# Kernel tuning notes

Measured on AMD Instinct MI355X. Metric: run time of the kernel, lower is better.

The kernel has to match this reference:

```python
import jax, jax.numpy as jnp
import numpy as np

RES = 300          # grid resolution per axis
NC_D = 16          # density_n_comp
NC_A = 48          # app_n_comp
APP_DIM = 27       # app_dim
N = 500000         # number of ray samples

MAT_MODE = [[0, 1], [0, 2], [1, 2]]
VEC_MODE = [2, 1, 0]


def setup_inputs() -> dict:
    key = jax.random.key(0)
    k0, k1, k2, k3 = jax.random.split(key, 4)
    xyz_sampled = jax.random.uniform(k0, (N, 3), minval=-1.0, maxval=1.0, dtype=jnp.float32)
    plane_coef = 0.1 * jax.random.normal(k1, (3, NC_A + NC_D, RES, RES), dtype=jnp.float32)
    line_coef = 0.1 * jax.random.normal(k2, (3, NC_A + NC_D, RES, 1), dtype=jnp.float32)
    basis_W = jax.random.normal(k3, (APP_DIM, 3 * NC_A), dtype=jnp.float32) / np.sqrt(3 * NC_A)
    return {"xyz_sampled": xyz_sampled, "plane_coef": plane_coef,
            "line_coef": line_coef, "basis_W": basis_W}


def _grid_sample(img, x, y):
    """Bilinear grid_sample, align_corners=True, zeros padding.
    img: (C, H, W); x, y: (N,) normalized coords in [-1, 1] (x -> W, y -> H).
    Returns (C, N)."""
    C, H, W = img.shape
    ix = (x + 1.0) * 0.5 * (W - 1)
    iy = (y + 1.0) * 0.5 * (H - 1)
    x0f = jnp.floor(ix)
    y0f = jnp.floor(iy)
    wx = ix - x0f   # weight for x0+1
    wy = iy - y0f   # weight for y0+1
    x0 = x0f.astype(jnp.int32)
    y0 = y0f.astype(jnp.int32)
    out = jnp.zeros((C, x.shape[0]), img.dtype)
    for dx, wxc in ((0, 1.0 - wx), (1, wx)):
        for dy, wyc in ((0, 1.0 - wy), (1, wy)):
            xi = x0 + dx
            yi = y0 + dy
            valid = (xi >= 0) & (xi < W) & (yi >= 0) & (yi < H)
            xic = jnp.clip(xi, 0, W - 1)
            yic = jnp.clip(yi, 0, H - 1)
            w = jnp.where(valid, wxc * wyc, 0.0)
            out = out + img[:, yic, xic] * w
    return out


def reference(xyz_sampled, plane_coef, line_coef, basis_W):
    zeros = jnp.zeros((xyz_sampled.shape[0],), xyz_sampled.dtype)
    pf, lf = [], []
    for i in range(3):
        m0, m1 = MAT_MODE[i]
        # plane: grid = (x=xyz[m0] -> W, y=xyz[m1] -> H)
        pf.append(_grid_sample(plane_coef[i], xyz_sampled[:, m0], xyz_sampled[:, m1]))
        # line: grid = (x=0 -> W(=1), y=xyz[vecMode] -> H) => 1D interp along H
        lf.append(_grid_sample(line_coef[i], zeros, xyz_sampled[:, VEC_MODE[i]]))
    pf = jnp.stack(pf)  # (3, NC_A+NC_D, N)
    lf = jnp.stack(lf)  # (3, NC_A+NC_D, N)
    # compute_densityfeature: last density_n_comp channels, multiply and sum-reduce
    sigma_feature = jnp.sum(pf[:, NC_A:] * lf[:, NC_A:], axis=(0, 1))  # (N,)
    # compute_appfeature: first app_n_comp channels, multiply then basis projection
    app_feats = (pf[:, :NC_A] * lf[:, :NC_A]).reshape(3 * NC_A, -1)    # (3*NC_A, N)
    app_features = app_feats.T @ basis_W.T                              # (N, APP_DIM)
    return sigma_feature, app_features
```

## Files before the change

kernel.cpp:

```cpp
#include <hip/hip_runtime.h>
#include <hip/hip_bf16.h>

#define RES 300
#define NPLANE (RES * RES)
#define NC_A 48
#define APP_DIM 27
#define KDIM 144
#define KS 168

#define NPBLK 4219

__device__ __forceinline__ float bf_lo(unsigned int u) { return __uint_as_float(u << 16); }
__device__ __forceinline__ float bf_hi(unsigned int u) { return __uint_as_float(u & 0xffff0000u); }

__global__ __launch_bounds__(256) void prep(
    const float* __restrict__ plane, const float* __restrict__ line,
    const float* __restrict__ W,
    uint2* __restrict__ TpV, unsigned int* __restrict__ TlP,
    __hip_bfloat16* __restrict__ Wg) {
  __shared__ unsigned int ltile[64 * 65];
  const int blk = blockIdx.x;
  const int tid = threadIdx.x;

  if (blk < NPBLK) {
    int flat = blk * 256 + tid;
    if (flat < 1080000) {
      int c4   = flat & 15;
      int rest = flat >> 4;
      int i  = (rest >= 45000) ? 2 : (rest >= 22500 ? 1 : 0);
      int p0 = (rest - i * 22500) * 4;
      const float* src = plane + (size_t)(i * 64 + c4 * 4) * NPLANE + p0;
      float4 r0 = *(const float4*)(src);
      float4 r1 = *(const float4*)(src + NPLANE);
      float4 r2 = *(const float4*)(src + 2 * NPLANE);
      float4 r3 = *(const float4*)(src + 3 * NPLANE);
      const float* rr[4] = {&r0.x, &r1.x, &r2.x, &r3.x};
      #pragma unroll
      for (int k = 0; k < 4; ++k) {
        __hip_bfloat162 h0, h1;
        h0.x = __float2bfloat16(rr[0][k]);
        h0.y = __float2bfloat16(rr[1][k]);
        h1.x = __float2bfloat16(rr[2][k]);
        h1.y = __float2bfloat16(rr[3][k]);
        uint2 u;
        u.x = *(unsigned int*)&h0;
        u.y = *(unsigned int*)&h1;
        TpV[((size_t)i * NPLANE + p0 + k) * 16 + c4] = u;
      }
    }
  } else if (blk < NPBLK + 15) {
    const int b  = blk - NPBLK;
    const int i  = b / 5;
    const int y0 = (b % 5) * 64;
    const int yl = tid & 63;
    const int cq = tid >> 6;
    #pragma unroll
    for (int k = 0; k < 16; ++k) {
      int c = cq * 16 + k;
      int y = y0 + yl;
      float a = 0.f, bv = 0.f;
      if (y < RES) {
        const float* row = line + (i * 64 + c) * RES;
        a  = row[y];
        bv = row[min(y + 1, RES - 1)];
      }
      __hip_bfloat162 h;
      h.x = __float2bfloat16(a);
      h.y = __float2bfloat16(bv);
      ltile[yl * 65 + c] = *(unsigned int*)&h;
    }
    __syncthreads();
    #pragma unroll
    for (int k = 0; k < 16; ++k) {
      int ylc = k * 4 + cq;
      int c   = tid & 63;
      int y   = y0 + ylc;
      if (y < RES) TlP[((size_t)i * RES + y) * 64 + c] = ltile[ylc * 65 + c];
    }
  } else {
    for (int idx = tid; idx < 2 * 5 * 64 * 8; idx += 256) {
      int j    = idx & 7;
      int lane = (idx >> 3) & 63;
      int kt   = (idx >> 9) % 5;
      int tile = idx / (5 * 64 * 8);
      int n = tile * 16 + (lane & 15);
      int k = kt * 32 + (lane >> 4) * 8 + j;
      float v = (n < APP_DIM && k < KDIM) ? W[n * KDIM + k] : 0.f;
      Wg[idx] = __float2bfloat16(v);
    }
  }
}

typedef __attribute__((ext_vector_type(8))) short short8;
typedef __attribute__((ext_vector_type(4))) float f32x4;

__global__ __launch_bounds__(256, 6) void tensorf_main(
    const float* __restrict__ xyz, const unsigned int* __restrict__ TpU,
    const unsigned int* __restrict__ TlP, const __hip_bfloat16* __restrict__ Wg,
    float* __restrict__ out, int n_total) {
  __shared__ __hip_bfloat16 prod[64 * KS];
  __shared__ float cw[64 * 18];

  const int tid  = threadIdx.x;
  const int lane = tid & 63;
  const int wave = tid >> 6;
  const int n0   = blockIdx.x * 64;

  for (int j = tid; j < 64 * 12; j += 256) {
    int s = j / 12, kk = (j % 12) * 2;
    *(unsigned int*)&prod[s * KS + KDIM + kk] = 0u;
  }

  if (tid < 64) {
    int n = min(n0 + tid, n_total - 1);
    float crd[3] = {xyz[3 * n], xyz[3 * n + 1], xyz[3 * n + 2]};
    const int m0s[3] = {0, 0, 1}, m1s[3] = {1, 2, 2}, vms[3] = {2, 1, 0};
    float* c = &cw[tid * 18];
    #pragma unroll
    for (int i = 0; i < 3; ++i) {
      float ix = fminf(fmaxf((crd[m0s[i]] + 1.f) * 149.5f, 0.f), 299.f);
      float iy = fminf(fmaxf((crd[m1s[i]] + 1.f) * 149.5f, 0.f), 299.f);
      float ly = fminf(fmaxf((crd[vms[i]] + 1.f) * 149.5f, 0.f), 299.f);
      float x0f = fminf(floorf(ix), 298.f);
      float y0f = fminf(floorf(iy), 298.f);
      float l0f = fminf(floorf(ly), 298.f);
      float wx = ix - x0f, wy = iy - y0f, lwy = ly - l0f;
      int cell = i * NPLANE + (int)y0f * RES + (int)x0f;
      int lidx = i * RES + (int)l0f;
      c[i * 6 + 0] = __int_as_float(cell | (lidx << 19));
      c[i * 6 + 1] = (1.f - wx) * (1.f - wy);
      c[i * 6 + 2] = wx * (1.f - wy);
      c[i * 6 + 3] = (1.f - wx) * wy;
      c[i * 6 + 4] = wx * wy;
      c[i * 6 + 5] = lwy;
    }
  }
  __syncthreads();

  const int cl   = lane & 31;
  const int half = lane >> 5;
  const int c2   = cl * 2;
  #pragma unroll 2
  for (int it = 0; it < 8; ++it) {
    int s = wave * 16 + it * 2 + half;
    const float* cp = &cw[s * 18];

    unsigned int u00[3], u01[3], u10[3], u11[3];
    uint2 ul[3];
    float wgt[3][5];
    #pragma unroll
    for (int i = 0; i < 3; ++i) {
      float2 q0 = *(const float2*)&cp[i * 6];
      float2 q1 = *(const float2*)&cp[i * 6 + 2];
      float2 q2 = *(const float2*)&cp[i * 6 + 4];
      int pk   = __float_as_int(q0.x);
      int cell = pk & 0x7FFFF;
      int lidx = pk >> 19;
      int bidx = cell * 32 + cl;
      u00[i] = TpU[bidx];
      u01[i] = TpU[bidx + 32];
      u10[i] = TpU[bidx + RES * 32];
      u11[i] = TpU[bidx + RES * 32 + 32];
      ul[i]  = *(const uint2*)&TlP[(lidx << 6) + c2];
      wgt[i][0] = q0.y; wgt[i][1] = q1.x; wgt[i][2] = q1.y;
      wgt[i][3] = q2.x; wgt[i][4] = q2.y;
    }

    float dsum = 0.f;
    #pragma unroll
    for (int i = 0; i < 3; ++i) {
      float pf_l = wgt[i][0] * bf_lo(u00[i]) + wgt[i][1] * bf_lo(u01[i]) +
                   wgt[i][2] * bf_lo(u10[i]) + wgt[i][3] * bf_lo(u11[i]);
      float pf_h = wgt[i][0] * bf_hi(u00[i]) + wgt[i][1] * bf_hi(u01[i]) +
                   wgt[i][2] * bf_hi(u10[i]) + wgt[i][3] * bf_hi(u11[i]);
      float lal = bf_lo(ul[i].x), lbl = bf_hi(ul[i].x);
      float lah = bf_lo(ul[i].y), lbh = bf_hi(ul[i].y);
      float lf_l = lal + wgt[i][4] * (lbl - lal);
      float lf_h = lah + wgt[i][4] * (lbh - lah);
      float prl = pf_l * lf_l, prh = pf_h * lf_h;
      if (cl < 24) {
        __hip_bfloat162 h;
        h.x = __float2bfloat16(prl);
        h.y = __float2bfloat16(prh);
        *(unsigned int*)&prod[s * KS + i * NC_A + c2] = *(unsigned int*)&h;
      } else {
        dsum += prl + prh;
      }
    }
    dsum += __shfl_xor(dsum, 1);
    dsum += __shfl_xor(dsum, 2);
    dsum += __shfl_xor(dsum, 4);
    int n = n0 + s;
    if (cl == 24 && n < n_total) out[n] = dsum;
  }
  __syncthreads();

  const int srow = lane & 15, quad = lane >> 4;
  f32x4 acc0 = {0.f, 0.f, 0.f, 0.f}, acc1 = {0.f, 0.f, 0.f, 0.f};
  const short* prodS = (const short*)prod;
  const short* WgS   = (const short*)Wg;
  const int arow = (wave * 16 + srow) * KS;
  #pragma unroll
  for (int kt = 0; kt < 5; ++kt) {
    short8 a  = *(const short8*)&prodS[arow + kt * 32 + quad * 8];
    short8 b0 = *(const short8*)&WgS[(kt * 64 + lane) * 8];
    short8 b1 = *(const short8*)&WgS[((5 + kt) * 64 + lane) * 8];
    acc0 = __builtin_amdgcn_mfma_f32_16x16x32_bf16(a, b0, acc0, 0, 0, 0);
    acc1 = __builtin_amdgcn_mfma_f32_16x16x32_bf16(a, b1, acc1, 0, 0, 0);
  }
  float* outApp = out + n_total;
  #pragma unroll
  for (int r = 0; r < 4; ++r) {
    int n = n0 + wave * 16 + quad * 4 + r;
    if (n < n_total) {
      outApp[(size_t)n * APP_DIM + srow] = acc0[r];
      if (srow < APP_DIM - 16)
        outApp[(size_t)n * APP_DIM + 16 + srow] = acc1[r];
    }
  }
}

extern "C" void kernel_launch(void* const* d_in, const int* in_sizes, int n_in,
                              void* d_out, int out_size, void* d_ws, size_t ws_size,
                              hipStream_t stream) {
  const float* xyz   = (const float*)d_in[0];
  const float* plane = (const float*)d_in[1];
  const float* line  = (const float*)d_in[2];
  const float* W     = (const float*)d_in[3];
  float* out = (float*)d_out;
  const int N = in_sizes[0] / 3;

  char* ws = (char*)d_ws;
  __hip_bfloat16* Tp  = (__hip_bfloat16*)ws;
  unsigned int*   TlP = (unsigned int*)(ws + 34560000);
  __hip_bfloat16* Wg  = (__hip_bfloat16*)(ws + 34560000 + 230400);

  prep<<<NPBLK + 16, 256, 0, stream>>>(plane, line, W, (uint2*)Tp, TlP, Wg);
  tensorf_main<<<(N + 63) / 64, 256, 0, stream>>>(
      xyz, (const unsigned int*)Tp, TlP, Wg, out, N);
}
```

Measured before the change: 227.6 us.

## Transpose plane prep through LDS and software-pipeline gathers in main kernel

The plane repack in prep now stages a 64-position by 64-channel tile in shared memory, so global writes become 16-byte rows instead of scattered 8-byte stores. The main kernel prefetches the next sample's bilinear gathers (double-buffered registers) while computing the current one, to hide gather latency. It also lowers the occupancy hint from 6 to 5 to make room for the extra registers. The doubled register footprint risks spills or fewer resident waves.

```diff
diff --git a/kernel.cpp b/kernel.cpp
--- a/kernel.cpp
+++ b/kernel.cpp
@@ -8,7 +8,8 @@
 #define KDIM 144
 #define KS 168
 
-#define NPBLK 4219
+#define PT_TILES 1407
+#define NPB2 (3 * PT_TILES)
 
 __device__ __forceinline__ float bf_lo(unsigned int u) { return __uint_as_float(u << 16); }
 __device__ __forceinline__ float bf_hi(unsigned int u) { return __uint_as_float(u & 0xffff0000u); }
@@ -16,40 +17,59 @@
 __global__ __launch_bounds__(256) void prep(
     const float* __restrict__ plane, const float* __restrict__ line,
     const float* __restrict__ W,
-    uint2* __restrict__ TpV, unsigned int* __restrict__ TlP,
+    unsigned int* __restrict__ TpUo, unsigned int* __restrict__ TlP,
     __hip_bfloat16* __restrict__ Wg) {
-  __shared__ unsigned int ltile[64 * 65];
+  __shared__ __align__(16) unsigned int lt[64 * 65];
   const int blk = blockIdx.x;
   const int tid = threadIdx.x;
 
-  if (blk < NPBLK) {
-    int flat = blk * 256 + tid;
-    if (flat < 1080000) {
-      int c4   = flat & 15;
-      int rest = flat >> 4;
-      int i  = (rest >= 45000) ? 2 : (rest >= 22500 ? 1 : 0);
-      int p0 = (rest - i * 22500) * 4;
-      const float* src = plane + (size_t)(i * 64 + c4 * 4) * NPLANE + p0;
-      float4 r0 = *(const float4*)(src);
-      float4 r1 = *(const float4*)(src + NPLANE);
-      float4 r2 = *(const float4*)(src + 2 * NPLANE);
-      float4 r3 = *(const float4*)(src + 3 * NPLANE);
-      const float* rr[4] = {&r0.x, &r1.x, &r2.x, &r3.x};
-      #pragma unroll
-      for (int k = 0; k < 4; ++k) {
-        __hip_bfloat162 h0, h1;
-        h0.x = __float2bfloat16(rr[0][k]);
-        h0.y = __float2bfloat16(rr[1][k]);
-        h1.x = __float2bfloat16(rr[2][k]);
-        h1.y = __float2bfloat16(rr[3][k]);
-        uint2 u;
-        u.x = *(unsigned int*)&h0;
-        u.y = *(unsigned int*)&h1;
-        TpV[((size_t)i * NPLANE + p0 + k) * 16 + c4] = u;
+  if (blk < NPB2) {
+    const int i  = blk / PT_TILES;
+    const int t0 = blk - i * PT_TILES;
+    const int p0 = t0 * 64;
+
+    const int cb   = (tid >> 4) * 4;
+    const int poff = (tid & 15) * 4;
+    const bool ok  = (p0 + poff) < NPLANE;
+
+    const float* src = plane + (size_t)(i * 64 + cb) * NPLANE + p0 + poff;
+    float4 v0, v1, v2, v3;
+    v0 = v1 = v2 = v3 = make_float4(0.f, 0.f, 0.f, 0.f);
+    if (ok) {
+      v0 = *(const float4*)(src);
+      v1 = *(const float4*)(src + NPLANE);
+      v2 = *(const float4*)(src + 2 * NPLANE);
+      v3 = *(const float4*)(src + 3 * NPLANE);
+    }
+    const int col = (tid >> 4) * 2;
+    const float* f0 = &v0.x; const float* f1 = &v1.x;
+    const float* f2 = &v2.x; const float* f3 = &v3.x;
+    #pragma unroll
+    for (int j = 0; j < 4; ++j) {
+      __hip_bfloat162 ha, hb;
+      ha.x = __float2bfloat16(f0[j]);
+      ha.y = __float2bfloat16(f1[j]);
+      hb.x = __float2bfloat16(f2[j]);
+      hb.y = __float2bfloat16(f3[j]);
+      uint2 u;
+      u.x = *(unsigned int*)&ha;
+      u.y = *(unsigned int*)&hb;
+      *(uint2*)&lt[(poff + j) * 34 + col] = u;
+    }
+    __syncthreads();
+    #pragma unroll
+    for (int pass = 0; pass < 2; ++pass) {
+      int p  = (tid >> 3) + pass * 32;
+      int c4 = (tid & 7) * 4;
+      if (p0 + p < NPLANE) {
+        uint2 a = *(const uint2*)&lt[p * 34 + c4];
+        uint2 b = *(const uint2*)&lt[p * 34 + c4 + 2];
+        uint4 w; w.x = a.x; w.y = a.y; w.z = b.x; w.w = b.y;
+        *(uint4*)&TpUo[((size_t)(i * NPLANE + p0 + p)) * 32 + c4] = w;
       }
     }
-  } else if (blk < NPBLK + 15) {
-    const int b  = blk - NPBLK;
+  } else if (blk < NPB2 + 15) {
+    const int b  = blk - NPB2;
     const int i  = b / 5;
     const int y0 = (b % 5) * 64;
     const int yl = tid & 63;
@@ -67,7 +87,7 @@
       __hip_bfloat162 h;
       h.x = __float2bfloat16(a);
       h.y = __float2bfloat16(bv);
-      ltile[yl * 65 + c] = *(unsigned int*)&h;
+      lt[yl * 65 + c] = *(unsigned int*)&h;
     }
     __syncthreads();
     #pragma unroll
@@ -75,7 +95,7 @@
       int ylc = k * 4 + cq;
       int c   = tid & 63;
       int y   = y0 + ylc;
-      if (y < RES) TlP[((size_t)i * RES + y) * 64 + c] = ltile[ylc * 65 + c];
+      if (y < RES) TlP[((size_t)i * RES + y) * 64 + c] = lt[ylc * 65 + c];
     }
   } else {
     for (int idx = tid; idx < 2 * 5 * 64 * 8; idx += 256) {
@@ -94,7 +114,35 @@
 typedef __attribute__((ext_vector_type(8))) short short8;
 typedef __attribute__((ext_vector_type(4))) float f32x4;
 
-__global__ __launch_bounds__(256, 6) void tensorf_main(
+struct Gather {
+  unsigned int u00[3], u01[3], u10[3], u11[3];
+  uint2 ul[3];
+  float w[3][5];
+};
+
+__device__ __forceinline__ void gather_it(
+    const float* __restrict__ cp, const unsigned int* __restrict__ TpU,
+    const unsigned int* __restrict__ TlP, int cl, int c2, Gather& g) {
+  #pragma unroll
+  for (int i = 0; i < 3; ++i) {
+    float2 q0 = *(const float2*)&cp[i * 6];
+    float2 q1 = *(const float2*)&cp[i * 6 + 2];
+    float2 q2 = *(const float2*)&cp[i * 6 + 4];
+    int pk   = __float_as_int(q0.x);
+    int cell = pk & 0x7FFFF;
+    int lidx = pk >> 19;
+    int bidx = cell * 32 + cl;
+    g.u00[i] = TpU[bidx];
+    g.u01[i] = TpU[bidx + 32];
+    g.u10[i] = TpU[bidx + RES * 32];
+    g.u11[i] = TpU[bidx + RES * 32 + 32];
+    g.ul[i]  = *(const uint2*)&TlP[(lidx << 6) + c2];
+    g.w[i][0] = q0.y; g.w[i][1] = q1.x; g.w[i][2] = q1.y;
+    g.w[i][3] = q2.x; g.w[i][4] = q2.y;
+  }
+}
+
+__global__ __launch_bounds__(256, 5) void tensorf_main(
     const float* __restrict__ xyz, const unsigned int* __restrict__ TpU,
     const unsigned int* __restrict__ TlP, const __hip_bfloat16* __restrict__ Wg,
     float* __restrict__ out, int n_total) {
@@ -140,43 +188,26 @@
   const int cl   = lane & 31;
   const int half = lane >> 5;
   const int c2   = cl * 2;
-  #pragma unroll 2
+
+  Gather cur, nxt;
+  gather_it(&cw[(wave * 16 + half) * 18], TpU, TlP, cl, c2, cur);
+  #pragma unroll
   for (int it = 0; it < 8; ++it) {
-    int s = wave * 16 + it * 2 + half;
-    const float* cp = &cw[s * 18];
-
-    unsigned int u00[3], u01[3], u10[3], u11[3];
-    uint2 ul[3];
-    float wgt[3][5];
+    const int s = wave * 16 + it * 2 + half;
+    if (it < 7)
+      gather_it(&cw[(s + 2) * 18], TpU, TlP, cl, c2, nxt);
+
+    float dsum = 0.f;
     #pragma unroll
     for (int i = 0; i < 3; ++i) {
-      float2 q0 = *(const float2*)&cp[i * 6];
-      float2 q1 = *(const float2*)&cp[i * 6 + 2];
-      float2 q2 = *(const float2*)&cp[i * 6 + 4];
-      int pk   = __float_as_int(q0.x);
-      int cell = pk & 0x7FFFF;
-      int lidx = pk >> 19;
-      int bidx = cell * 32 + cl;
-      u00[i] = TpU[bidx];
-      u01[i] = TpU[bidx + 32];
-      u10[i] = TpU[bidx + RES * 32];
-      u11[i] = TpU[bidx + RES * 32 + 32];
-      ul[i]  = *(const uint2*)&TlP[(lidx << 6) + c2];
-      wgt[i][0] = q0.y; wgt[i][1] = q1.x; wgt[i][2] = q1.y;
-      wgt[i][3] = q2.x; wgt[i][4] = q2.y;
-    }
-
-    float dsum = 0.f;
-    #pragma unroll
-    for (int i = 0; i < 3; ++i) {
-      float pf_l = wgt[i][0] * bf_lo(u00[i]) + wgt[i][1] * bf_lo(u01[i]) +
-                   wgt[i][2] * bf_lo(u10[i]) + wgt[i][3] * bf_lo(u11[i]);
-      float pf_h = wgt[i][0] * bf_hi(u00[i]) + wgt[i][1] * bf_hi(u01[i]) +
-                   wgt[i][2] * bf_hi(u10[i]) + wgt[i][3] * bf_hi(u11[i]);
-      float lal = bf_lo(ul[i].x), lbl = bf_hi(ul[i].x);
-      float lah = bf_lo(ul[i].y), lbh = bf_hi(ul[i].y);
-      float lf_l = lal + wgt[i][4] * (lbl - lal);
-      float lf_h = lah + wgt[i][4] * (lbh - lah);
+      float pf_l = cur.w[i][0] * bf_lo(cur.u00[i]) + cur.w[i][1] * bf_lo(cur.u01[i]) +
+                   cur.w[i][2] * bf_lo(cur.u10[i]) + cur.w[i][3] * bf_lo(cur.u11[i]);
+      float pf_h = cur.w[i][0] * bf_hi(cur.u00[i]) + cur.w[i][1] * bf_hi(cur.u01[i]) +
+                   cur.w[i][2] * bf_hi(cur.u10[i]) + cur.w[i][3] * bf_hi(cur.u11[i]);
+      float lal = bf_lo(cur.ul[i].x), lbl = bf_hi(cur.ul[i].x);
+      float lah = bf_lo(cur.ul[i].y), lbh = bf_hi(cur.ul[i].y);
+      float lf_l = lal + cur.w[i][4] * (lbl - lal);
+      float lf_h = lah + cur.w[i][4] * (lbh - lah);
       float prl = pf_l * lf_l, prh = pf_h * lf_h;
       if (cl < 24) {
         __hip_bfloat162 h;
@@ -192,6 +223,7 @@
     dsum += __shfl_xor(dsum, 4);
     int n = n0 + s;
     if (cl == 24 && n < n_total) out[n] = dsum;
+    if (it < 7) cur = nxt;
   }
   __syncthreads();
 
@@ -235,7 +267,7 @@
   unsigned int*   TlP = (unsigned int*)(ws + 34560000);
   __hip_bfloat16* Wg  = (__hip_bfloat16*)(ws + 34560000 + 230400);
 
-  prep<<<NPBLK + 16, 256, 0, stream>>>(plane, line, W, (uint2*)Tp, TlP, Wg);
+  prep<<<NPB2 + 16, 256, 0, stream>>>(plane, line, W, (unsigned int*)Tp, TlP, Wg);
   tensorf_main<<<(N + 63) / 64, 256, 0, stream>>>(
       xyz, (const unsigned int*)Tp, TlP, Wg, out, N);
 }
```

After: 227.1 us. About the same (-0.2%).
